# Optimization experiments

Hardware: AMD Instinct MI355X
Metric: run time of the kernel (lower is better)

Reference implementation:

```python
import jax, jax.numpy as jnp
import numpy as np

B, N, D = 8, 2048, 1024

def setup_inputs() -> dict:
    key = jax.random.key(0)
    ks = jax.random.split(key, 4)
    x = jax.random.normal(ks[0], (B, N, D), dtype=jnp.float32)
    # Glorot-uniform-like scaling as keras Dense default
    def glorot(k, shape):
        fan_in, fan_out = shape[0], shape[1]
        lim = jnp.sqrt(6.0 / (fan_in + fan_out)).astype(jnp.float32)
        return jax.random.uniform(k, shape, jnp.float32, -lim, lim)
    Wq = glorot(ks[1], (D, D))
    Wk = glorot(ks[2], (D, D))
    Wout = glorot(ks[3], (N, D))  # out_proj acts on last axis of [B,N,N] scores
    bq = jnp.zeros((D,), jnp.float32)
    bk = jnp.zeros((D,), jnp.float32)
    bout = jnp.zeros((D,), jnp.float32)
    return {"x": x, "Wq": Wq, "bq": bq, "Wk": Wk, "bk": bk, "Wout": Wout, "bout": bout}

def reference(x, Wq, bq, Wk, bk, Wout, bout):
    Q = x @ Wq + bq                                  # [B,N,D]
    K = x @ Wk + bk                                  # [B,N,D]
    scores = jnp.einsum("bnd,bmd->bnm", Q, K)       # [B,N,N] (no 1/sqrt(d) in source)
    A = jax.nn.softmax(scores, axis=-1)              # [B,N,N]
    return A @ Wout + bout                           # [B,N,D]
```

## Files before the change

### kernel.cpp

```cpp
#include <hip/hip_runtime.h>


typedef unsigned short u16;
typedef __bf16 bf16x8 __attribute__((ext_vector_type(8)));
typedef float f32x4 __attribute__((ext_vector_type(4)));

#define BB 8
#define NN 2048
#define DD 1024
#define MT (BB * NN)
#define PSTRIDE 4096

#define MFMA3(d, ah, al, bh, bl)                                         \
  d = __builtin_amdgcn_mfma_f32_16x16x32_bf16(ah, bh, d, 0, 0, 0);       \
  d = __builtin_amdgcn_mfma_f32_16x16x32_bf16(ah, bl, d, 0, 0, 0);       \
  d = __builtin_amdgcn_mfma_f32_16x16x32_bf16(al, bh, d, 0, 0, 0);

static __device__ __forceinline__ u16 f2bf(float f) {
  unsigned u = __builtin_bit_cast(unsigned, f);
  u += 0x7FFFu + ((u >> 16) & 1u);
  return (u16)(u >> 16);
}
static __device__ __forceinline__ float bf2f(u16 h) {
  unsigned u = ((unsigned)h) << 16;
  return __builtin_bit_cast(float, u);
}

static __device__ __forceinline__ void gload16(const void* g, void* l) {
  __builtin_amdgcn_global_load_lds((const __attribute__((address_space(1))) void*)g,
                                   (__attribute__((address_space(3))) void*)l, 16, 0, 0);
}

static __device__ __forceinline__ int swz_wg() {
  int nwg = gridDim.x;
  int orig = blockIdx.x;
  int q = nwg >> 3;
  return (orig & 7) * q + (orig >> 3);
}

#define SW(r) (((r) ^ ((r) >> 2)) & 3)

static __device__ __forceinline__ void stage_plane_sw(const u16* __restrict__ g0,
                                                      u16* lp0, int tid, int ld) {
#pragma unroll
  for (int j = 0; j < 2; j++) {
    int o = tid + j * 512;
    int row = o >> 2, c = o & 3;
    const u16* g = g0 + (size_t)row * ld + ((c ^ SW(row)) << 3);
    u16* lp = lp0 + (((tid >> 6) << 6) + j * 512) * 8;
    gload16(g, lp);
  }
}

static __device__ __forceinline__ void stage_half_sw(const u16* __restrict__ g0,
                                                     u16* lp0, int tid, int ld) {
  int o = tid;
  int row = o >> 2, c = o & 3;
  const u16* g = g0 + (size_t)row * ld + ((c ^ SW(row)) << 3);
  u16* lp = lp0 + ((tid >> 6) << 6) * 8;
  gload16(g, lp);
}

static __device__ __forceinline__ bf16x8 rdfrag(const u16* plane, int row, int g4) {
  return *(const bf16x8*)&plane[row * 32 + ((g4 ^ SW(row)) << 3)];
}

template <bool STG, int VM>
static __device__ __forceinline__ void tile4(
    u16* Lc, const u16* Ah, const u16* Al, const u16* Bh, const u16* Bl, int kst,
    f32x4 (&acc)[8][4], int tid, int wm, int wn, int r16, int g4) {
  u16* PA0 = Lc;
  u16* PA1 = Lc + 8192;
  u16* PB0 = Lc + 16384;
  u16* PB1 = Lc + 24576;
  bf16x8 a0[4], a1[4], b0[4], b1[4];

#pragma unroll
  for (int fm = 0; fm < 4; fm++) {
    int rw = wm * 128 + fm * 16 + r16;
    a0[fm] = rdfrag(PA0, rw, g4);
    a1[fm] = rdfrag(PA1, rw, g4);
  }
#pragma unroll
  for (int fn = 0; fn < 2; fn++) {
    int rw = wn * 64 + fn * 16 + r16;
    b0[fn] = rdfrag(PB0, rw, g4);
    b1[fn] = rdfrag(PB1, rw, g4);
  }
  __builtin_amdgcn_s_barrier();
  asm volatile("s_waitcnt lgkmcnt(0)" ::: "memory");
  __builtin_amdgcn_s_setprio(1);
#pragma unroll
  for (int fm = 0; fm < 4; fm++)
#pragma unroll
    for (int fn = 0; fn < 2; fn++) { MFMA3(acc[fm][fn], a0[fm], a1[fm], b0[fn], b1[fn]); }
  __builtin_amdgcn_s_setprio(0);

#pragma unroll
  for (int fn = 2; fn < 4; fn++) {
    int rw = wn * 64 + fn * 16 + r16;
    b0[fn] = rdfrag(PB0, rw, g4);
    b1[fn] = rdfrag(PB1, rw, g4);
  }
  __builtin_amdgcn_s_barrier();
  asm volatile("s_waitcnt lgkmcnt(0)" ::: "memory");
  __builtin_amdgcn_s_setprio(1);
#pragma unroll
  for (int fm = 0; fm < 4; fm++)
#pragma unroll
    for (int fn = 2; fn < 4; fn++) { MFMA3(acc[fm][fn], a0[fm], a1[fm], b0[fn], b1[fn]); }
  __builtin_amdgcn_s_setprio(0);
  __builtin_amdgcn_s_barrier();

#pragma unroll
  for (int fm = 0; fm < 4; fm++) {
    int rw = wm * 128 + 64 + fm * 16 + r16;
    a0[fm] = rdfrag(PA0, rw, g4);
    a1[fm] = rdfrag(PA1, rw, g4);
  }
  if (STG) {
    stage_plane_sw(Bh + kst, PB0, tid, DD);
    stage_plane_sw(Bl + kst, PB1, tid, DD);
  }
  __builtin_amdgcn_s_barrier();
  asm volatile("s_waitcnt lgkmcnt(0)" ::: "memory");
  __builtin_amdgcn_s_setprio(1);
#pragma unroll
  for (int fm = 0; fm < 4; fm++)
#pragma unroll
    for (int fn = 0; fn < 2; fn++) { MFMA3(acc[fm + 4][fn], a0[fm], a1[fm], b0[fn], b1[fn]); }
  __builtin_amdgcn_s_setprio(0);
  __builtin_amdgcn_s_barrier();

  if (STG) {
    stage_plane_sw(Ah + kst, PA0, tid, DD);
    stage_plane_sw(Al + kst, PA1, tid, DD);
  }
  if (VM == 8) {
    asm volatile("s_waitcnt vmcnt(8)" ::: "memory");
  } else if (VM == 0) {
    asm volatile("s_waitcnt vmcnt(0)" ::: "memory");
  }
  __builtin_amdgcn_s_barrier();
  __builtin_amdgcn_s_setprio(1);
#pragma unroll
  for (int fm = 0; fm < 4; fm++)
#pragma unroll
    for (int fn = 2; fn < 4; fn++) { MFMA3(acc[fm + 4][fn], a0[fm], a1[fm], b0[fn], b1[fn]); }
  __builtin_amdgcn_s_setprio(0);
}

static __device__ __forceinline__ void mm8_core(u16* L, const u16* Ah, const u16* Al,
                                                const u16* Bh, const u16* Bl,
                                                f32x4 (&acc)[8][4], int tid) {
  int lane = tid & 63, r16 = lane & 15, g4 = lane >> 4;
  int w = tid >> 6, wm = w >> 2, wn = w & 3;
  u16* L0 = L;
  u16* L1 = L + 4 * 8192;
  stage_plane_sw(Ah + 0, L0 + 0, tid, DD);
  stage_plane_sw(Al + 0, L0 + 8192, tid, DD);
  stage_plane_sw(Bh + 0, L0 + 16384, tid, DD);
  stage_plane_sw(Bl + 0, L0 + 24576, tid, DD);
  stage_plane_sw(Ah + 32, L1 + 0, tid, DD);
  stage_plane_sw(Al + 32, L1 + 8192, tid, DD);
  stage_plane_sw(Bh + 32, L1 + 16384, tid, DD);
  stage_plane_sw(Bl + 32, L1 + 24576, tid, DD);
  asm volatile("s_waitcnt vmcnt(8)" ::: "memory");
  __builtin_amdgcn_s_barrier();
#pragma unroll 1
  for (int i = 0; i < 15; i++) {
    int t0 = 2 * i;
    tile4<true, 8>(L0, Ah, Al, Bh, Bl, (t0 + 2) * 32, acc, tid, wm, wn, r16, g4);
    tile4<true, 8>(L1, Ah, Al, Bh, Bl, (t0 + 3) * 32, acc, tid, wm, wn, r16, g4);
  }
  tile4<false, 0>(L0, Ah, Al, Bh, Bl, 0, acc, tid, wm, wn, r16, g4);
  tile4<false, -1>(L1, Ah, Al, Bh, Bl, 0, acc, tid, wm, wn, r16, g4);
}

__launch_bounds__(512, 2)
__global__ void k_gemm_s8(const u16* __restrict__ yh, const u16* __restrict__ yl,
                          const u16* __restrict__ xh, const u16* __restrict__ xl,
                          float* __restrict__ S) {
  __shared__ __attribute__((aligned(16))) u16 lds[2][4][8192];
  int wg = swz_wg();
  int nt = wg & 7, mtot = wg >> 3;
  int b = mtot >> 3, mt = mtot & 7;
  const size_t po = (size_t)b * NN * DD;
  const u16* Ah = yh + po + (size_t)(mt * 256) * DD;
  const u16* Al = yl + po + (size_t)(mt * 256) * DD;
  const u16* Bh = xh + po + (size_t)(nt * 256) * DD;
  const u16* Bl = xl + po + (size_t)(nt * 256) * DD;
  int tid = threadIdx.x;
  f32x4 acc[8][4] = {};
  mm8_core(&lds[0][0][0], Ah, Al, Bh, Bl, acc, tid);
  int lane = tid & 63, r16 = lane & 15, g4 = lane >> 4;
  int w = tid >> 6, wm = w >> 2, wn = w & 3;
  float* Sb = S + (size_t)b * NN * NN;
#pragma unroll
  for (int fm = 0; fm < 8; fm++)
#pragma unroll
    for (int fn = 0; fn < 4; fn++) {
      int col = nt * 256 + wn * 64 + fn * 16 + r16;
      int row = mt * 256 + wm * 128 + fm * 16 + g4 * 4;
#pragma unroll
      for (int i2 = 0; i2 < 4; i2++)
        Sb[(size_t)(row + i2) * NN + col] = acc[fm][fn][i2];
    }
}

__launch_bounds__(512, 2)
__global__ void k_gemm_y8(const u16* __restrict__ ah_g, const u16* __restrict__ al_g,
                          const u16* __restrict__ bh_g, const u16* __restrict__ bl_g,
                          u16* __restrict__ ohi, u16* __restrict__ olo) {
  __shared__ __attribute__((aligned(16))) u16 lds[2][4][8192];
  int wg = swz_wg();
  int nt = wg & 3, mt = wg >> 2;
  const u16* Ah = ah_g + (size_t)(mt * 256) * DD;
  const u16* Al = al_g + (size_t)(mt * 256) * DD;
  const u16* Bh = bh_g + (size_t)(nt * 256) * DD;
  const u16* Bl = bl_g + (size_t)(nt * 256) * DD;
  int tid = threadIdx.x;
  f32x4 acc[8][4] = {};
  mm8_core(&lds[0][0][0], Ah, Al, Bh, Bl, acc, tid);
  int lane = tid & 63, r16 = lane & 15, g4 = lane >> 4;
  int w = tid >> 6, wm = w >> 2, wn = w & 3;
#pragma unroll
  for (int fm = 0; fm < 8; fm++)
#pragma unroll
    for (int fn = 0; fn < 4; fn++) {
      int col = nt * 256 + wn * 64 + fn * 16 + r16;
      int row = mt * 256 + wm * 128 + fm * 16 + g4 * 4;
#pragma unroll
      for (int i2 = 0; i2 < 4; i2++) {
        float v = acc[fm][fn][i2];
        u16 h = f2bf(v);
        size_t o = (size_t)(row + i2) * DD + col;
        ohi[o] = h;
        olo[o] = f2bf(v - bf2f(h));
      }
    }
}

static __device__ __forceinline__ void stage128_lin(const u16* __restrict__ g0,
                                                    u16* lp0, int tid, int ld) {
#pragma unroll
  for (int j = 0; j < 2; j++) {
    int o = tid + j * 256;
    const u16* g = g0 + (size_t)(o >> 2) * ld + (o & 3) * 8;
    u16* lp = lp0 + (((tid >> 6) << 6) + j * 256) * 8;
    gload16(g, lp);
  }
}

__launch_bounds__(256)
__global__ void k_gemm_mt(const u16* __restrict__ wkh, const u16* __restrict__ wkl,
                          const u16* __restrict__ wqh, const u16* __restrict__ wql,
                          float* __restrict__ part) {
  __shared__ __attribute__((aligned(16))) u16 lds[4][128][32];
  int idx = blockIdx.x;
  int ks = idx >> 6, mt = (idx >> 3) & 7, nt = idx & 7;
  int t = threadIdx.x, lane = t & 63, w = t >> 6;
  int wr = w >> 1, wc = w & 1, r16 = lane & 15, g = lane >> 4;
  const u16* Ah = wkh + (size_t)(mt * 128) * DD;
  const u16* Al = wkl + (size_t)(mt * 128) * DD;
  const u16* Bh = wqh + (size_t)(nt * 128) * DD;
  const u16* Bl = wql + (size_t)(nt * 128) * DD;
  float* P = part + (size_t)ks * DD * DD;

  f32x4 acc[4][4] = {};
  for (int k0 = ks * 256; k0 < ks * 256 + 256; k0 += 32) {
    stage128_lin(Ah + k0, &lds[0][0][0], t, DD);
    stage128_lin(Al + k0, &lds[1][0][0], t, DD);
    stage128_lin(Bh + k0, &lds[2][0][0], t, DD);
    stage128_lin(Bl + k0, &lds[3][0][0], t, DD);
    asm volatile("s_waitcnt vmcnt(0)" ::: "memory");
    __syncthreads();
    bf16x8 bh[4], bl[4];
#pragma unroll
    for (int fn = 0; fn < 4; fn++) {
      int col = wc * 64 + fn * 16 + r16;
      bh[fn] = *(const bf16x8*)&lds[2][col][g * 8];
      bl[fn] = *(const bf16x8*)&lds[3][col][g * 8];
    }
#pragma unroll
    for (int fm = 0; fm < 4; fm++) {
      int row = wr * 64 + fm * 16 + r16;
      bf16x8 ah = *(const bf16x8*)&lds[0][row][g * 8];
      bf16x8 al = *(const bf16x8*)&lds[1][row][g * 8];
#pragma unroll
      for (int fn = 0; fn < 4; fn++) { MFMA3(acc[fm][fn], ah, al, bh[fn], bl[fn]); }
    }
    __syncthreads();
  }
#pragma unroll
  for (int fm = 0; fm < 4; fm++)
#pragma unroll
    for (int fn = 0; fn < 4; fn++) {
      int col = nt * 128 + wc * 64 + fn * 16 + r16;
      int row = mt * 128 + wr * 64 + fm * 16 + g * 4;
#pragma unroll
      for (int i = 0; i < 4; i++)
        P[(size_t)(row + i) * DD + col] = acc[fm][fn][i];
    }
}

__global__ void k_combine_split(const float* __restrict__ part, u16* __restrict__ hi,
                                u16* __restrict__ lo) {
  const long n4 = (long)DD * DD / 4;
  long i = (long)blockIdx.x * blockDim.x + threadIdx.x;
  long stride = (long)gridDim.x * blockDim.x;
  const float4* p0 = (const float4*)part;
  const float4* p1 = (const float4*)(part + (size_t)DD * DD);
  const float4* p2 = (const float4*)(part + (size_t)2 * DD * DD);
  const float4* p3 = (const float4*)(part + (size_t)3 * DD * DD);
  for (; i < n4; i += stride) {
    float4 a = p0[i], b = p1[i], c = p2[i], d = p3[i];
    float4 v;
    v.x = a.x + b.x + c.x + d.x;
    v.y = a.y + b.y + c.y + d.y;
    v.z = a.z + b.z + c.z + d.z;
    v.w = a.w + b.w + c.w + d.w;
    u16 h0 = f2bf(v.x), h1 = f2bf(v.y), h2 = f2bf(v.z), h3 = f2bf(v.w);
    ushort4 hv; hv.x = h0; hv.y = h1; hv.z = h2; hv.w = h3;
    ushort4 lv;
    lv.x = f2bf(v.x - bf2f(h0)); lv.y = f2bf(v.y - bf2f(h1));
    lv.z = f2bf(v.z - bf2f(h2)); lv.w = f2bf(v.w - bf2f(h3));
    ((ushort4*)hi)[i] = hv;
    ((ushort4*)lo)[i] = lv;
  }
}

template <bool STG, int VM>
static __device__ __forceinline__ void tile4q(
    u16* Lc, const u16* Ag, const u16* Bg, int kst,
    f32x4 (&acc)[4][4], int tid, int wm, int wn, int r16, int g4) {
  u16* PA = Lc;
  u16* PB = Lc + 8192;
  bf16x8 a4[4], b4[4];

#pragma unroll
  for (int fm = 0; fm < 2; fm++) a4[fm] = rdfrag(PA, wm * 64 + fm * 16 + r16, g4);
#pragma unroll
  for (int fn = 0; fn < 2; fn++) b4[fn] = rdfrag(PB, wn * 64 + fn * 16 + r16, g4);
  __builtin_amdgcn_s_barrier();
  asm volatile("s_waitcnt lgkmcnt(0)" ::: "memory");
  __builtin_amdgcn_s_setprio(1);
#pragma unroll
  for (int fm = 0; fm < 2; fm++)
#pragma unroll
    for (int fn = 0; fn < 2; fn++)
      acc[fm][fn] = __builtin_amdgcn_mfma_f32_16x16x32_bf16(a4[fm], b4[fn], acc[fm][fn], 0, 0, 0);
  __builtin_amdgcn_s_setprio(0);

#pragma unroll
  for (int fn = 2; fn < 4; fn++) b4[fn] = rdfrag(PB, wn * 64 + fn * 16 + r16, g4);
  __builtin_amdgcn_s_barrier();
  asm volatile("s_waitcnt lgkmcnt(0)" ::: "memory");
  __builtin_amdgcn_s_setprio(1);
#pragma unroll
  for (int fm = 0; fm < 2; fm++)
#pragma unroll
    for (int fn = 2; fn < 4; fn++)
      acc[fm][fn] = __builtin_amdgcn_mfma_f32_16x16x32_bf16(a4[fm], b4[fn], acc[fm][fn], 0, 0, 0);
  __builtin_amdgcn_s_setprio(0);
  __builtin_amdgcn_s_barrier();

#pragma unroll
  for (int fm = 2; fm < 4; fm++) a4[fm] = rdfrag(PA, wm * 64 + fm * 16 + r16, g4);
  if (STG) stage_half_sw(Bg + kst, PB, tid, NN);
  __builtin_amdgcn_s_barrier();
  asm volatile("s_waitcnt lgkmcnt(0)" ::: "memory");
  __builtin_amdgcn_s_setprio(1);
#pragma unroll
  for (int fm = 2; fm < 4; fm++)
#pragma unroll
    for (int fn = 0; fn < 2; fn++)
      acc[fm][fn] = __builtin_amdgcn_mfma_f32_16x16x32_bf16(a4[fm], b4[fn], acc[fm][fn], 0, 0, 0);
  __builtin_amdgcn_s_setprio(0);
  __builtin_amdgcn_s_barrier();

  if (STG) stage_plane_sw(Ag + kst, PA, tid, PSTRIDE);
  if (VM == 3) {
    asm volatile("s_waitcnt vmcnt(3)" ::: "memory");
  } else if (VM == 0) {
    asm volatile("s_waitcnt vmcnt(0)" ::: "memory");
  }
  __builtin_amdgcn_s_barrier();
  __builtin_amdgcn_s_setprio(1);
#pragma unroll
  for (int fm = 2; fm < 4; fm++)
#pragma unroll
    for (int fn = 2; fn < 4; fn++)
      acc[fm][fn] = __builtin_amdgcn_mfma_f32_16x16x32_bf16(a4[fm], b4[fn], acc[fm][fn], 0, 0, 0);
  __builtin_amdgcn_s_setprio(0);
}

__launch_bounds__(512, 2)
__global__ void k_gemm_out(const u16* __restrict__ P, const u16* __restrict__ woutT,
                           const float* __restrict__ bout, float* __restrict__ out) {
  __shared__ __attribute__((aligned(16))) u16 lds[2][12288];
  int wg = swz_wg();
  int b = wg >> 6, mt = (wg >> 3) & 7, nt = wg & 7;
  const u16* Ag = P + (size_t)b * NN * PSTRIDE + (size_t)(mt * 256) * PSTRIDE;
  const u16* Bg = woutT + (size_t)(nt * 128) * NN;
  float* ob = out + (size_t)b * NN * DD;

  int tid = threadIdx.x;
  int lane = tid & 63, r16 = lane & 15, g4 = lane >> 4;
  int w = tid >> 6, wm = w >> 1, wn = w & 1;
  u16* L0 = &lds[0][0];
  u16* L1 = &lds[1][0];

  f32x4 acc[4][4] = {};
  stage_plane_sw(Ag + 0, L0, tid, PSTRIDE);
  stage_half_sw(Bg + 0, L0 + 8192, tid, NN);
  stage_plane_sw(Ag + 32, L1, tid, PSTRIDE);
  stage_half_sw(Bg + 32, L1 + 8192, tid, NN);
  asm volatile("s_waitcnt vmcnt(3)" ::: "memory");
  __builtin_amdgcn_s_barrier();
#pragma unroll 1
  for (int i = 0; i < 31; i++) {
    int t0 = 2 * i;
    tile4q<true, 3>(L0, Ag, Bg, (t0 + 2) * 32, acc, tid, wm, wn, r16, g4);
    tile4q<true, 3>(L1, Ag, Bg, (t0 + 3) * 32, acc, tid, wm, wn, r16, g4);
  }
  tile4q<false, 0>(L0, Ag, Bg, 0, acc, tid, wm, wn, r16, g4);
  tile4q<false, -1>(L1, Ag, Bg, 0, acc, tid, wm, wn, r16, g4);

#pragma unroll
  for (int fm = 0; fm < 4; fm++)
#pragma unroll
    for (int fn = 0; fn < 4; fn++) {
      int col = nt * 128 + wn * 64 + fn * 16 + r16;
      float bv = bout[col];
      int row = mt * 256 + wm * 64 + fm * 16 + g4 * 4;
#pragma unroll
      for (int i2 = 0; i2 < 4; i2++)
        ob[(size_t)(row + i2) * DD + col] = acc[fm][fn][i2] + bv;
    }
}

__global__ void k_split(const float* __restrict__ x, u16* __restrict__ hi,
                        u16* __restrict__ lo, long n4) {
  long i = (long)blockIdx.x * blockDim.x + threadIdx.x;
  long stride = (long)gridDim.x * blockDim.x;
  for (; i < n4; i += stride) {
    float4 v = ((const float4*)x)[i];
    u16 h0 = f2bf(v.x), h1 = f2bf(v.y), h2 = f2bf(v.z), h3 = f2bf(v.w);
    ushort4 hv; hv.x = h0; hv.y = h1; hv.z = h2; hv.w = h3;
    ushort4 lv;
    lv.x = f2bf(v.x - bf2f(h0)); lv.y = f2bf(v.y - bf2f(h1));
    lv.z = f2bf(v.z - bf2f(h2)); lv.w = f2bf(v.w - bf2f(h3));
    ((ushort4*)hi)[i] = hv;
    ((ushort4*)lo)[i] = lv;
  }
}

__global__ void k_split_x(const float* __restrict__ x, const float* __restrict__ v2,
                          u16* __restrict__ hi, u16* __restrict__ lo,
                          float* __restrict__ c2) {
  int w = threadIdx.x >> 6, lane = threadIdx.x & 63;
  int row = blockIdx.x * 4 + w;
  const float4* xr = (const float4*)(x + (size_t)row * DD);
  const float4* vv = (const float4*)v2;
  ushort4* hr = (ushort4*)(hi + (size_t)row * DD);
  ushort4* lr = (ushort4*)(lo + (size_t)row * DD);
  float s = 0.f;
#pragma unroll
  for (int j = 0; j < 4; j++) {
    int idx = j * 64 + lane;
    float4 v = xr[idx];
    float4 b = vv[idx];
    s += v.x * b.x + v.y * b.y + v.z * b.z + v.w * b.w;
    u16 h0 = f2bf(v.x), h1 = f2bf(v.y), h2 = f2bf(v.z), h3 = f2bf(v.w);
    ushort4 hv; hv.x = h0; hv.y = h1; hv.z = h2; hv.w = h3;
    ushort4 lv;
    lv.x = f2bf(v.x - bf2f(h0)); lv.y = f2bf(v.y - bf2f(h1));
    lv.z = f2bf(v.z - bf2f(h2)); lv.w = f2bf(v.w - bf2f(h3));
    hr[idx] = hv;
    lr[idx] = lv;
  }
#pragma unroll
  for (int o = 32; o > 0; o >>= 1) s += __shfl_xor(s, o);
  if (lane == 0) c2[row] = s;
}

__global__ void k_transpose_split(const float* __restrict__ W, u16* __restrict__ thi,
                                  int R, int C) {
  __shared__ float tile[32][33];
  int c0 = blockIdx.x * 32, r0 = blockIdx.y * 32;
  int tx = threadIdx.x, ty = threadIdx.y;
#pragma unroll
  for (int i = 0; i < 4; i++)
    tile[ty + i * 8][tx] = W[(size_t)(r0 + ty + i * 8) * C + c0 + tx];
  __syncthreads();
#pragma unroll
  for (int i = 0; i < 4; i++) {
    float v = tile[tx][ty + i * 8];
    thi[(size_t)(c0 + ty + i * 8) * R + r0 + tx] = f2bf(v);
  }
}

__global__ void k_matvec(const float* __restrict__ A, const float* __restrict__ v,
                         float* __restrict__ out, int cols) {
  int w = threadIdx.x >> 6, lane = threadIdx.x & 63;
  int row = blockIdx.x * 4 + w;
  const float4* Ar = (const float4*)(A + (size_t)row * cols);
  const float4* vv = (const float4*)v;
  float s = 0.f;
  for (int j = lane; j < cols / 4; j += 64) {
    float4 a = Ar[j], b = vv[j];
    s += a.x * b.x + a.y * b.y + a.z * b.z + a.w * b.w;
  }
#pragma unroll
  for (int o = 32; o > 0; o >>= 1) s += __shfl_xor(s, o);
  if (lane == 0) out[row] = s;
}

__global__ void k_softmax(float* __restrict__ S, const float* __restrict__ c2, int nrows) {
  int w = threadIdx.x >> 6, lane = threadIdx.x & 63;
  int row = blockIdx.x * 4 + w;
  if (row >= nrows) return;
  const float4* Sr = (const float4*)(S + (size_t)row * NN);
  const float4* c2b = (const float4*)(c2 + ((size_t)(row >> 11) << 11));
  float4 v[8];
  float mx = -3.4e38f;
#pragma unroll
  for (int j = 0; j < 8; j++) {
    v[j] = Sr[j * 64 + lane];
    float4 c = c2b[j * 64 + lane];
    v[j].x += c.x; v[j].y += c.y; v[j].z += c.z; v[j].w += c.w;
    mx = fmaxf(mx, fmaxf(fmaxf(v[j].x, v[j].y), fmaxf(v[j].z, v[j].w)));
  }
#pragma unroll
  for (int o = 32; o > 0; o >>= 1) mx = fmaxf(mx, __shfl_xor(mx, o));
  float e[32];
  float sum = 0.f;
#pragma unroll
  for (int j = 0; j < 8; j++) {
    e[j * 4 + 0] = __expf(v[j].x - mx);
    e[j * 4 + 1] = __expf(v[j].y - mx);
    e[j * 4 + 2] = __expf(v[j].z - mx);
    e[j * 4 + 3] = __expf(v[j].w - mx);
    sum += e[j * 4 + 0] + e[j * 4 + 1] + e[j * 4 + 2] + e[j * 4 + 3];
  }
#pragma unroll
  for (int o = 32; o > 0; o >>= 1) sum += __shfl_xor(sum, o);
  float inv = 1.0f / sum;
  ushort4* Pr = (ushort4*)((u16*)S + (size_t)row * PSTRIDE);
#pragma unroll
  for (int j = 0; j < 8; j++) {
    ushort4 pv;
    pv.x = f2bf(e[j * 4 + 0] * inv);
    pv.y = f2bf(e[j * 4 + 1] * inv);
    pv.z = f2bf(e[j * 4 + 2] * inv);
    pv.w = f2bf(e[j * 4 + 3] * inv);
    Pr[j * 64 + lane] = pv;
  }
}

extern "C" void kernel_launch(void* const* d_in, const int* in_sizes, int n_in,
                              void* d_out, int out_size, void* d_ws, size_t ws_size,
                              hipStream_t stream) {
  const float* x = (const float*)d_in[0];
  const float* Wq = (const float*)d_in[1];
  const float* bq = (const float*)d_in[2];
  const float* Wk = (const float*)d_in[3];
  const float* bk = (const float*)d_in[4];
  const float* Wout = (const float*)d_in[5];
  const float* bout = (const float*)d_in[6];
  float* out = (float*)d_out;
  char* ws = (char*)d_ws;

  const size_t MB = 1ull << 20;
  u16* mth = (u16*)(ws + 0 * MB);
  u16* mtl = (u16*)(ws + 2 * MB);
  u16* woutT = (u16*)(ws + 4 * MB);
  float* v2 = (float*)(ws + 8 * MB);
  float* c2 = (float*)(ws + 8 * MB + 65536);
  char* base = ws + 12 * MB;

  dim3 tb(32, 8, 1);

  if (ws_size >= 204 * MB) {
    u16* xh = (u16*)(base);
    u16* xl = (u16*)(base + 32 * MB);
    u16* yh = (u16*)(base + 64 * MB);
    u16* yl = (u16*)(base + 96 * MB);
    char* R = base + 128 * MB;
    u16* wqh = (u16*)(R);
    u16* wql = (u16*)(R + 2 * MB);
    u16* wkh = (u16*)(R + 4 * MB);
    u16* wkl = (u16*)(R + 6 * MB);
    float* mtp = (float*)(R + 8 * MB);
    float* S = (float*)R;

    k_split<<<256, 256, 0, stream>>>(Wq, wqh, wql, (long)DD * DD / 4);
    k_split<<<256, 256, 0, stream>>>(Wk, wkh, wkl, (long)DD * DD / 4);
    k_gemm_mt<<<256, 256, 0, stream>>>(wkh, wkl, wqh, wql, mtp);
    k_combine_split<<<256, 256, 0, stream>>>(mtp, mth, mtl);
    k_transpose_split<<<dim3(32, 64, 1), tb, 0, stream>>>(Wout, woutT, 2048, 1024);
    k_matvec<<<256, 256, 0, stream>>>(Wk, bq, v2, DD);
    k_split_x<<<MT / 4, 256, 0, stream>>>(x, v2, xh, xl, c2);
    k_gemm_y8<<<256, 512, 0, stream>>>(xh, xl, mth, mtl, yh, yl);
    for (int h = 0; h < 2; h++) {
      size_t qo = (size_t)h * 4 * NN * DD;
      k_gemm_s8<<<256, 512, 0, stream>>>(yh + qo, yl + qo, xh + qo, xl + qo, S);
      k_softmax<<<4 * NN / 4, 256, 0, stream>>>(S, c2 + (size_t)h * 4 * NN, 4 * NN);
      k_gemm_out<<<256, 512, 0, stream>>>((const u16*)S, woutT, bout, out + qo);
    }
  } else if (ws_size >= 156 * MB) {
    u16* xh = (u16*)(base);
    u16* xl = (u16*)(base + 32 * MB);
    u16* yh = (u16*)(base + 64 * MB);
    u16* yl = (u16*)(base + 96 * MB);
    char* R = base + 128 * MB;
    u16* wqh = (u16*)(R);
    u16* wql = (u16*)(R + 2 * MB);
    u16* wkh = (u16*)(R + 4 * MB);
    u16* wkl = (u16*)(R + 6 * MB);
    float* mtp = (float*)yh;
    float* S = (float*)R;

    k_split<<<256, 256, 0, stream>>>(Wq, wqh, wql, (long)DD * DD / 4);
    k_split<<<256, 256, 0, stream>>>(Wk, wkh, wkl, (long)DD * DD / 4);
    k_gemm_mt<<<256, 256, 0, stream>>>(wkh, wkl, wqh, wql, mtp);
    k_combine_split<<<256, 256, 0, stream>>>(mtp, mth, mtl);
    k_transpose_split<<<dim3(32, 64, 1), tb, 0, stream>>>(Wout, woutT, 2048, 1024);
    k_matvec<<<256, 256, 0, stream>>>(Wk, bq, v2, DD);
    k_split_x<<<MT / 4, 256, 0, stream>>>(x, v2, xh, xl, c2);
    k_gemm_y8<<<256, 512, 0, stream>>>(xh, xl, mth, mtl, yh, yl);
    for (int b = 0; b < BB; b++) {
      size_t qo = (size_t)b * NN * DD;
      k_gemm_s8<<<64, 512, 0, stream>>>(yh + qo, yl + qo, xh + qo, xl + qo, S);
      k_softmax<<<NN / 4, 256, 0, stream>>>(S, c2 + (size_t)b * NN, NN);
      k_gemm_out<<<64, 512, 0, stream>>>((const u16*)S, woutT, bout, out + qo);
    }
  } else {
    u16* xh = (u16*)(base);
    u16* xl = (u16*)(base + 8 * MB);
    u16* yh = (u16*)(base + 16 * MB);
    u16* yl = (u16*)(base + 24 * MB);
    char* R = base + 32 * MB;
    u16* wqh = (u16*)(R);
    u16* wql = (u16*)(R + 2 * MB);
    u16* wkh = (u16*)(R + 4 * MB);
    u16* wkl = (u16*)(R + 6 * MB);
    float* mtp = (float*)yh;
    float* S = (float*)R;

    k_split<<<256, 256, 0, stream>>>(Wq, wqh, wql, (long)DD * DD / 4);
    k_split<<<256, 256, 0, stream>>>(Wk, wkh, wkl, (long)DD * DD / 4);
    k_gemm_mt<<<256, 256, 0, stream>>>(wkh, wkl, wqh, wql, mtp);
    k_combine_split<<<256, 256, 0, stream>>>(mtp, mth, mtl);
    k_transpose_split<<<dim3(32, 64, 1), tb, 0, stream>>>(Wout, woutT, 2048, 1024);
    k_matvec<<<256, 256, 0, stream>>>(Wk, bq, v2, DD);
    for (int c = 0; c < 4; c++) {
      size_t xo = (size_t)c * 2 * NN * DD;
      k_split_x<<<2 * NN / 4, 256, 0, stream>>>(x + xo, v2, xh, xl, c2 + (size_t)c * 2 * NN);
      k_gemm_y8<<<64, 512, 0, stream>>>(xh, xl, mth, mtl, yh, yl);
      for (int bi = 0; bi < 2; bi++) {
        size_t lo = (size_t)bi * NN * DD;
        k_gemm_s8<<<64, 512, 0, stream>>>(yh + lo, yl + lo, xh + lo, xl + lo, S);
        k_softmax<<<NN / 4, 256, 0, stream>>>(S, c2 + (size_t)(c * 2 + bi) * NN, NN);
        k_gemm_out<<<64, 512, 0, stream>>>((const u16*)S, woutT, bout, out + xo + lo);
      }
    }
  }
}
```

Before: 438.6 us.

## Retile Y projection GEMM to 128x128 tiles with 256-thread blocks and start skew

```diff
diff --git a/kernel.cpp b/kernel.cpp
--- a/kernel.cpp
+++ b/kernel.cpp
@@ -36,6 +36,13 @@
   int orig = blockIdx.x;
   int q = nwg >> 3;
   return (orig & 7) * q + (orig >> 3);
+}
+
+static __device__ __forceinline__ void skew_spin() {
+  unsigned h = (unsigned)blockIdx.x * 2654435761u;
+  long long cyc = (long long)((h >> 16) & 4095u);
+  long long t0 = clock64();
+  while (clock64() - t0 < cyc) {}
 }
 
 #define SW(r) (((r) ^ ((r) >> 2)) & 3)
@@ -59,6 +66,18 @@
   const u16* g = g0 + (size_t)row * ld + ((c ^ SW(row)) << 3);
   u16* lp = lp0 + ((tid >> 6) << 6) * 8;
   gload16(g, lp);
+}
+
+static __device__ __forceinline__ void stage_p128(const u16* __restrict__ g0,
+                                                  u16* lp0, int tid, int ld) {
+#pragma unroll
+  for (int j = 0; j < 2; j++) {
+    int o = tid + j * 256;
+    int row = o >> 2, c = o & 3;
+    const u16* g = g0 + (size_t)row * ld + ((c ^ SW(row)) << 3);
+    u16* lp = lp0 + (((tid >> 6) << 6) + j * 256) * 8;
+    gload16(g, lp);
+  }
 }
 
 static __device__ __forceinline__ bf16x8 rdfrag(const u16* plane, int row, int g4) {
@@ -208,28 +227,115 @@
     }
 }
 
-__launch_bounds__(512, 2)
+template <bool STG, int VM>
+static __device__ __forceinline__ void tile128(
+    u16* Lc, const u16* Ah, const u16* Al, const u16* Bh, const u16* Bl, int kst,
+    f32x4 (&acc)[4][4], int tid, int wr, int wc, int r16, int g4) {
+  u16* PA0 = Lc;
+  u16* PA1 = Lc + 4096;
+  u16* PB0 = Lc + 8192;
+  u16* PB1 = Lc + 12288;
+  bf16x8 a0[4], a1[4], b0[4], b1[4];
+
+#pragma unroll
+  for (int fm = 0; fm < 4; fm++) {
+    int rw = wr * 64 + fm * 16 + r16;
+    a0[fm] = rdfrag(PA0, rw, g4);
+    a1[fm] = rdfrag(PA1, rw, g4);
+  }
+#pragma unroll
+  for (int fn = 0; fn < 2; fn++) {
+    int rw = wc * 64 + fn * 16 + r16;
+    b0[fn] = rdfrag(PB0, rw, g4);
+    b1[fn] = rdfrag(PB1, rw, g4);
+  }
+  asm volatile("s_waitcnt lgkmcnt(0)" ::: "memory");
+  __builtin_amdgcn_s_setprio(1);
+#pragma unroll
+  for (int fm = 0; fm < 4; fm++)
+#pragma unroll
+    for (int fn = 0; fn < 2; fn++) { MFMA3(acc[fm][fn], a0[fm], a1[fm], b0[fn], b1[fn]); }
+  __builtin_amdgcn_s_setprio(0);
+
+#pragma unroll
+  for (int fn = 2; fn < 4; fn++) {
+    int rw = wc * 64 + fn * 16 + r16;
+    b0[fn] = rdfrag(PB0, rw, g4);
+    b1[fn] = rdfrag(PB1, rw, g4);
+  }
+  asm volatile("s_waitcnt lgkmcnt(0)" ::: "memory");
+  __builtin_amdgcn_s_setprio(1);
+#pragma unroll
+  for (int fm = 0; fm < 4; fm++)
+#pragma unroll
+    for (int fn = 2; fn < 4; fn++) { MFMA3(acc[fm][fn], a0[fm], a1[fm], b0[fn], b1[fn]); }
+  __builtin_amdgcn_s_setprio(0);
+  __builtin_amdgcn_s_barrier();
+
+  if (STG) {
+    stage_p128(Ah + kst, PA0, tid, DD);
+    stage_p128(Al + kst, PA1, tid, DD);
+    stage_p128(Bh + kst, PB0, tid, DD);
+    stage_p128(Bl + kst, PB1, tid, DD);
+  }
+  if (VM == 8) {
+    asm volatile("s_waitcnt vmcnt(8)" ::: "memory");
+  } else if (VM == 0) {
+    asm volatile("s_waitcnt vmcnt(0)" ::: "memory");
+  }
+  __builtin_amdgcn_s_barrier();
+}
+
+static __device__ __forceinline__ void mm4_core(u16* L, const u16* Ah, const u16* Al,
+                                                const u16* Bh, const u16* Bl,
+                                                f32x4 (&acc)[4][4], int tid) {
+  int lane = tid & 63, r16 = lane & 15, g4 = lane >> 4;
+  int w = tid >> 6, wr = w >> 1, wc = w & 1;
+  u16* L0 = L;
+  u16* L1 = L + 16384;
+  stage_p128(Ah + 0, L0 + 0, tid, DD);
+  stage_p128(Al + 0, L0 + 4096, tid, DD);
+  stage_p128(Bh + 0, L0 + 8192, tid, DD);
+  stage_p128(Bl + 0, L0 + 12288, tid, DD);
+  stage_p128(Ah + 32, L1 + 0, tid, DD);
+  stage_p128(Al + 32, L1 + 4096, tid, DD);
+  stage_p128(Bh + 32, L1 + 8192, tid, DD);
+  stage_p128(Bl + 32, L1 + 12288, tid, DD);
+  asm volatile("s_waitcnt vmcnt(8)" ::: "memory");
+  __builtin_amdgcn_s_barrier();
+#pragma unroll 1
+  for (int i = 0; i < 15; i++) {
+    int t0 = 2 * i;
+    tile128<true, 8>(L0, Ah, Al, Bh, Bl, (t0 + 2) * 32, acc, tid, wr, wc, r16, g4);
+    tile128<true, 8>(L1, Ah, Al, Bh, Bl, (t0 + 3) * 32, acc, tid, wr, wc, r16, g4);
+  }
+  tile128<false, 0>(L0, Ah, Al, Bh, Bl, 0, acc, tid, wr, wc, r16, g4);
+  tile128<false, -1>(L1, Ah, Al, Bh, Bl, 0, acc, tid, wr, wc, r16, g4);
+}
+
+__launch_bounds__(256, 2)
 __global__ void k_gemm_y8(const u16* __restrict__ ah_g, const u16* __restrict__ al_g,
                           const u16* __restrict__ bh_g, const u16* __restrict__ bl_g,
                           u16* __restrict__ ohi, u16* __restrict__ olo) {
-  __shared__ __attribute__((aligned(16))) u16 lds[2][4][8192];
+  __shared__ __attribute__((aligned(16))) u16 lds[2][4][4096];
   int wg = swz_wg();
-  int nt = wg & 3, mt = wg >> 2;
-  const u16* Ah = ah_g + (size_t)(mt * 256) * DD;
-  const u16* Al = al_g + (size_t)(mt * 256) * DD;
-  const u16* Bh = bh_g + (size_t)(nt * 256) * DD;
-  const u16* Bl = bl_g + (size_t)(nt * 256) * DD;
+  int nt = wg & 7, mt = wg >> 3;
+  const u16* Ah = ah_g + (size_t)(mt * 128) * DD;
+  const u16* Al = al_g + (size_t)(mt * 128) * DD;
+  const u16* Bh = bh_g + (size_t)(nt * 128) * DD;
+  const u16* Bl = bl_g + (size_t)(nt * 128) * DD;
   int tid = threadIdx.x;
-  f32x4 acc[8][4] = {};
-  mm8_core(&lds[0][0][0], Ah, Al, Bh, Bl, acc, tid);
+  skew_spin();
+  f32x4 acc[4][4] = {};
+  mm4_core(&lds[0][0][0], Ah, Al, Bh, Bl, acc, tid);
   int lane = tid & 63, r16 = lane & 15, g4 = lane >> 4;
-  int w = tid >> 6, wm = w >> 2, wn = w & 3;
-#pragma unroll
-  for (int fm = 0; fm < 8; fm++)
+  int w = tid >> 6, wr = w >> 1, wc = w & 1;
+#pragma unroll
+  for (int fm = 0; fm < 4; fm++)
 #pragma unroll
     for (int fn = 0; fn < 4; fn++) {
-      int col = nt * 256 + wn * 64 + fn * 16 + r16;
-      int row = mt * 256 + wm * 128 + fm * 16 + g4 * 4;
+      int col = nt * 128 + wc * 64 + fn * 16 + r16;
+      int row = mt * 128 + wr * 64 + fm * 16 + g4 * 4;
 #pragma unroll
       for (int i2 = 0; i2 < 4; i2++) {
         float v = acc[fm][fn][i2];
@@ -602,7 +708,7 @@
     k_transpose_split<<<dim3(32, 64, 1), tb, 0, stream>>>(Wout, woutT, 2048, 1024);
     k_matvec<<<256, 256, 0, stream>>>(Wk, bq, v2, DD);
     k_split_x<<<MT / 4, 256, 0, stream>>>(x, v2, xh, xl, c2);
-    k_gemm_y8<<<256, 512, 0, stream>>>(xh, xl, mth, mtl, yh, yl);
+    k_gemm_y8<<<1024, 256, 0, stream>>>(xh, xl, mth, mtl, yh, yl);
     for (int h = 0; h < 2; h++) {
       size_t qo = (size_t)h * 4 * NN * DD;
       k_gemm_s8<<<256, 512, 0, stream>>>(yh + qo, yl + qo, xh + qo, xl + qo, S);
@@ -629,7 +735,7 @@
     k_transpose_split<<<dim3(32, 64, 1), tb, 0, stream>>>(Wout, woutT, 2048, 1024);
     k_matvec<<<256, 256, 0, stream>>>(Wk, bq, v2, DD);
     k_split_x<<<MT / 4, 256, 0, stream>>>(x, v2, xh, xl, c2);
-    k_gemm_y8<<<256, 512, 0, stream>>>(xh, xl, mth, mtl, yh, yl);
+    k_gemm_y8<<<1024, 256, 0, stream>>>(xh, xl, mth, mtl, yh, yl);
     for (int b = 0; b < BB; b++) {
       size_t qo = (size_t)b * NN * DD;
       k_gemm_s8<<<64, 512, 0, stream>>>(yh + qo, yl + qo, xh + qo, xl + qo, S);
@@ -658,7 +764,7 @@
     for (int c = 0; c < 4; c++) {
       size_t xo = (size_t)c * 2 * NN * DD;
       k_split_x<<<2 * NN / 4, 256, 0, stream>>>(x + xo, v2, xh, xl, c2 + (size_t)c * 2 * NN);
-      k_gemm_y8<<<64, 512, 0, stream>>>(xh, xl, mth, mtl, yh, yl);
+      k_gemm_y8<<<256, 256, 0, stream>>>(xh, xl, mth, mtl, yh, yl);
       for (int bi = 0; bi < 2; bi++) {
         size_t lo = (size_t)bi * NN * DD;
         k_gemm_s8<<<64, 512, 0, stream>>>(yh + lo, yl + lo, xh + lo, xl + lo, S);
```

Measured after the change: 449.1 us. +2.4%, slower.
